# Kernel optimization log

Measured on AMD Instinct MI355X. Metric: run time of the kernel, lower is better.

## Reference

```python
import jax, jax.numpy as jnp
import numpy as np

# FP4 E2M1 value table (codes 0..7 positive, 8..15 negative, sign in MSB)
FP4_VALUES = jnp.array([0.0, 0.5, 1.0, 1.5, 2.0, 3.0, 4.0, 6.0,
                        -0.0, -0.5, -1.0, -1.5, -2.0, -3.0, -4.0, -6.0],
                       dtype=jnp.float32)


def setup_inputs() -> dict:
    key = jax.random.key(0)
    k1, k2, k3, k4 = jax.random.split(key, 4)
    O, I = 4096, 4096
    block = 16
    x = jax.random.normal(k1, (8192, I), dtype=jnp.float32)
    # packed uint4 pairs stored as int32 bytes in [0, 256)
    weight = jax.random.randint(k2, (O, I // 2), 0, 256, dtype=jnp.int32)
    # per-block FP8-style scales (positive)
    weight_scale = jax.random.uniform(k3, (O, I // block), dtype=jnp.float32, minval=0.01, maxval=1.0)
    bias = jax.random.normal(k4, (O,), dtype=jnp.float32)
    return {"x": x, "weight": weight, "weight_scale": weight_scale,
            "bias": bias, "block_size": block}


def _dequant_nvfp4(weight, weight_scale, block_size):
    # unpack two FP4 codes per byte: high nibble is the even (first) element
    hi = (weight >> 4) & 0xF
    lo = weight & 0xF
    O = weight.shape[0]
    codes = jnp.stack([hi, lo], axis=-1).reshape(O, -1)  # [O, I]
    vals = FP4_VALUES[codes]                             # [O, I] f32
    I = vals.shape[1]
    # apply per-block scale
    w = vals.reshape(O, I // block_size, block_size) * weight_scale[:, :, None]
    return w.reshape(O, I)


def reference(x, weight, weight_scale, bias, block_size):
    w = _dequant_nvfp4(weight, weight_scale, block_size)  # [O, I]
    return jnp.einsum('ti,oi->to', x, w) + bias[None, :]
```

## Files before the change

kernel.cpp:

```cpp
#include <hip/hip_runtime.h>
#include <hip/hip_fp16.h>

typedef __attribute__((ext_vector_type(8))) _Float16 f16x8;
typedef __attribute__((ext_vector_type(4))) float f32x4;

#define M_DIM 8192
#define N_DIM 4096
#define K_DIM 4096
#define BM 256
#define BN 256
#define BK 64
#define NT (K_DIM / BK)
#define ITERS (NT / 2)

__constant__ float FP4_LUT[16] = {0.f, 0.5f, 1.f, 1.5f, 2.f, 3.f, 4.f, 6.f,
                                  -0.f, -0.5f, -1.f, -1.5f, -2.f, -3.f, -4.f, -6.f};

__device__ inline void glds16(const void* g, void* l) {
    __builtin_amdgcn_global_load_lds(
        (const __attribute__((address_space(1))) void*)g,
        (__attribute__((address_space(3))) void*)l, 16, 0, 0);
}

__global__ __launch_bounds__(256) void prep_kernel(const float* __restrict__ x,
                                                   _Float16* __restrict__ xh,
                                                   const int* __restrict__ w,
                                                   const float* __restrict__ wsc,
                                                   _Float16* __restrict__ wh) {
    int b = blockIdx.x;
    if (b < 16384) {
        int i = (b * 256 + threadIdx.x) * 8;
        const float4* p = (const float4*)(x + i);
        float4 a = p[0], c = p[1];
        f16x8 h;
        h[0] = (_Float16)a.x; h[1] = (_Float16)a.y;
        h[2] = (_Float16)a.z; h[3] = (_Float16)a.w;
        h[4] = (_Float16)c.x; h[5] = (_Float16)c.y;
        h[6] = (_Float16)c.z; h[7] = (_Float16)c.w;
        *(f16x8*)(xh + i) = h;
    } else {
        int t = (b - 16384) * 256 + threadIdx.x;
        int4 b4 = ((const int4*)w)[t];
        int o  = t >> 9;
        int j0 = (t & 511) << 2;
        float s = wsc[(o << 8) + (j0 >> 3)];
        f16x8 h;
        int v;
        v = b4.x; h[0] = (_Float16)(FP4_LUT[(v >> 4) & 15] * s); h[1] = (_Float16)(FP4_LUT[v & 15] * s);
        v = b4.y; h[2] = (_Float16)(FP4_LUT[(v >> 4) & 15] * s); h[3] = (_Float16)(FP4_LUT[v & 15] * s);
        v = b4.z; h[4] = (_Float16)(FP4_LUT[(v >> 4) & 15] * s); h[5] = (_Float16)(FP4_LUT[v & 15] * s);
        v = b4.w; h[6] = (_Float16)(FP4_LUT[(v >> 4) & 15] * s); h[7] = (_Float16)(FP4_LUT[v & 15] * s);
        *(f16x8*)(wh + ((long)o << 12) + (j0 << 1)) = h;
    }
}


#define VM4 asm volatile("s_waitcnt vmcnt(4)" ::: "memory")
#define VM0 asm volatile("s_waitcnt vmcnt(0)" ::: "memory")
#define LG8 asm volatile("s_waitcnt lgkmcnt(8)" ::: "memory")
#define LG4 asm volatile("s_waitcnt lgkmcnt(4)" ::: "memory")
#define LG0 asm volatile("s_waitcnt lgkmcnt(0)" ::: "memory")
#define NOP ((void)0)

#define STAGE(OP, SD, KH, KOFF) do {                                           \
    _Float16* _d = lds + (SD)*32768 + (OP)*16384 + (KH)*8192 + (wid << 9);     \
    const _Float16* _s = ((OP) ? srcB : srcA) + (KOFF);                        \
    glds16(_s, _d);                                                            \
    glds16(_s + (size_t)128 * K_DIM, _d + 4096);                               \
  } while (0)

#define PH(DOAF, NCB, NKH, NMH, AFN, DOBF, BFN, LGW, MHC, AFC, BFC, STG, VMW, BAR) do { \
    STG;                                                                       \
    const _Float16* _nb = lds + (NCB)*32768 + (NKH)*8192;                      \
    if (DOAF) {                                                                \
      AFN[0] = *(const f16x8*)(_nb + a_off + (NMH)*2048);                      \
      AFN[1] = *(const f16x8*)(_nb + a_off + (NMH)*2048 + 512);                \
      AFN[2] = *(const f16x8*)(_nb + a_off + (NMH)*2048 + 1024);               \
      AFN[3] = *(const f16x8*)(_nb + a_off + (NMH)*2048 + 1536);               \
    }                                                                          \
    if (DOBF) {                                                                \
      BFN[0] = *(const f16x8*)(_nb + b_off);                                   \
      BFN[1] = *(const f16x8*)(_nb + b_off + 512);                             \
      BFN[2] = *(const f16x8*)(_nb + b_off + 1024);                            \
      BFN[3] = *(const f16x8*)(_nb + b_off + 1536);                            \
    }                                                                          \
    LGW;                                                                       \
    __builtin_amdgcn_s_setprio(1);                                             \
    _Pragma("unroll")                                                          \
    for (int mf = 0; mf < 4; ++mf) {                                           \
      _Pragma("unroll")                                                        \
      for (int nf = 0; nf < 4; ++nf)                                           \
        acc[(MHC)*4 + mf][nf] = __builtin_amdgcn_mfma_f32_16x16x32_f16(        \
            AFC[mf], BFC[nf], acc[(MHC)*4 + mf][nf], 0, 0, 0);                 \
    }                                                                          \
    __builtin_amdgcn_s_setprio(0);                                             \
    VMW;                                                                       \
    if (BAR) __builtin_amdgcn_s_barrier();                                     \
  } while (0)

__global__ __launch_bounds__(512, 2) void gemm_f16_pf(const _Float16* __restrict__ A,
                                                      const _Float16* __restrict__ B,
                                                      const float* __restrict__ bias,
                                                      float* __restrict__ C) {
    __shared__ _Float16 lds[2 * 32768];

    const int tid  = threadIdx.x;
    const int wid  = tid >> 6;
    const int lane = tid & 63;
    const int fr   = lane & 15;
    const int kg   = lane >> 4;
    const int wm   = wid >> 2;
    const int wn   = wid & 3;

    const int c = blockIdx.x & 7;
    const int q = blockIdx.x >> 3;
    const int bm = (c >> 1) * 8 + (q & 7);
    const int bn = (c & 1) * 8 + (q >> 3);
    const int brow = bm * BM;
    const int bcol = bn * BN;

    const int s_col = (((tid & 3) ^ ((tid >> 3) & 3)) << 3);
    const _Float16* srcA = A + (size_t)(brow + (tid >> 2)) * K_DIM + s_col;
    const _Float16* srcB = B + (size_t)(bcol + (tid >> 2)) * K_DIM + s_col;

    const int swz   = ((kg ^ ((fr >> 1) & 3)) << 3);
    const int a_off = (wm * 128 + fr) * 32 + swz;
    const int b_off = 16384 + (wn * 64 + fr) * 32 + swz;

    f16x8 af0[4], af1[4], bf0[4], bf1[4];
    f32x4 acc[8][4] = {};

    STAGE(0, 0, 0, 0);
    STAGE(1, 0, 0, 0);
    STAGE(0, 0, 1, 32);
    STAGE(1, 0, 1, 32);
    STAGE(0, 1, 0, 64);
    STAGE(1, 1, 0, 64);
    VM4;
    __builtin_amdgcn_s_barrier();
    af0[0] = *(const f16x8*)(lds + a_off);
    af0[1] = *(const f16x8*)(lds + a_off + 512);
    af0[2] = *(const f16x8*)(lds + a_off + 1024);
    af0[3] = *(const f16x8*)(lds + a_off + 1536);
    bf0[0] = *(const f16x8*)(lds + b_off);
    bf0[1] = *(const f16x8*)(lds + b_off + 512);
    bf0[2] = *(const f16x8*)(lds + b_off + 1024);
    bf0[3] = *(const f16x8*)(lds + b_off + 1536);

    for (int i = 0; i < ITERS - 1; ++i) {
        const int kb = i << 7;
        PH(1, 0,0,1, af1, 0,bf0, LG4, 0, af0, bf0, STAGE(0,1,1,kb+96),  NOP, 0);
        PH(1, 0,1,0, af0, 1,bf1, LG8, 1, af1, bf0, STAGE(1,1,1,kb+96),  VM4, 1);
        PH(1, 0,1,1, af1, 0,bf0, LG4, 0, af0, bf1, STAGE(0,0,0,kb+128), NOP, 0);
        PH(1, 1,0,0, af0, 1,bf0, LG8, 1, af1, bf1, STAGE(1,0,0,kb+128), VM4, 1);
        PH(1, 1,0,1, af1, 0,bf0, LG4, 0, af0, bf0, STAGE(0,0,1,kb+160), NOP, 0);
        PH(1, 1,1,0, af0, 1,bf1, LG8, 1, af1, bf0, STAGE(1,0,1,kb+160), VM4, 1);
        PH(1, 1,1,1, af1, 0,bf0, LG4, 0, af0, bf1, STAGE(0,1,0,kb+192), NOP, 0);
        PH(1, 0,0,0, af0, 1,bf0, LG8, 1, af1, bf1, STAGE(1,1,0,kb+192), VM4, 1);
    }
    {
        const int kb = (ITERS - 1) << 7;
        PH(1, 0,0,1, af1, 0,bf0, LG4, 0, af0, bf0, STAGE(0,1,1,kb+96), NOP, 0);
        PH(1, 0,1,0, af0, 1,bf1, LG8, 1, af1, bf0, STAGE(1,1,1,kb+96), VM4, 1);
        PH(1, 0,1,1, af1, 0,bf0, LG4, 0, af0, bf1, NOP,                NOP, 0);
        PH(1, 1,0,0, af0, 1,bf0, LG8, 1, af1, bf1, NOP,                VM0, 1);
        PH(1, 1,0,1, af1, 0,bf0, LG4, 0, af0, bf0, NOP,                NOP, 0);
        PH(1, 1,1,0, af0, 1,bf1, LG8, 1, af1, bf0, NOP,                NOP, 1);
        PH(1, 1,1,1, af1, 0,bf0, LG4, 0, af0, bf1, NOP,                NOP, 0);
        PH(0, 0,0,0, af0, 0,bf0, LG0, 1, af1, bf1, NOP,                NOP, 0);
    }

#pragma unroll
    for (int m = 0; m < 8; ++m) {
        int row = brow + wm * 128 + m * 16 + kg * 4;
#pragma unroll
        for (int n = 0; n < 4; ++n) {
            int col = bcol + wn * 64 + n * 16 + fr;
            float bv = bias[col];
#pragma unroll
            for (int j = 0; j < 4; ++j)
                C[(size_t)(row + j) * N_DIM + col] = acc[m][n][j] + bv;
        }
    }
}

__global__ __launch_bounds__(256) void fallback_kernel(const float* __restrict__ x,
                                                       const int* __restrict__ w,
                                                       const float* __restrict__ wsc,
                                                       const float* __restrict__ bias,
                                                       float* __restrict__ out) {
    long idx = (long)blockIdx.x * 256 + threadIdx.x;
    int t = (int)(idx >> 12);
    int o = (int)(idx & 4095);
    float acc = 0.f;
    for (int j = 0; j < K_DIM / 2; ++j) {
        int b = w[o * (K_DIM / 2) + j];
        float s = wsc[(o << 8) + (j >> 3)];
        acc += x[(long)t * K_DIM + 2 * j]     * (FP4_LUT[(b >> 4) & 15] * s);
        acc += x[(long)t * K_DIM + 2 * j + 1] * (FP4_LUT[b & 15] * s);
    }
    out[idx] = acc + bias[o];
}

extern "C" void kernel_launch(void* const* d_in, const int* in_sizes, int n_in,
                              void* d_out, int out_size, void* d_ws, size_t ws_size,
                              hipStream_t stream) {
    const float* x    = (const float*)d_in[0];
    const int*   w    = (const int*)d_in[1];
    const float* wsc  = (const float*)d_in[2];
    const float* bias = (const float*)d_in[3];
    float* out = (float*)d_out;

    const size_t xh_bytes = (size_t)M_DIM * K_DIM * 2;
    const size_t wh_bytes = (size_t)N_DIM * K_DIM * 2;

    if (ws_size >= xh_bytes + wh_bytes) {
        _Float16* xh = (_Float16*)d_ws;
        _Float16* wh = (_Float16*)((char*)d_ws + xh_bytes);
        prep_kernel<<<16384 + 8192, 256, 0, stream>>>(x, xh, w, wsc, wh);
        gemm_f16_pf<<<(M_DIM / BM) * (N_DIM / BN), 512, 0, stream>>>(xh, wh, bias, out);
    } else {
        fallback_kernel<<<((long)M_DIM * N_DIM) / 256, 256, 0, stream>>>(x, w, wsc, bias, out);
    }
}
```

Measured before the change: 276.6 us.

## Switch GEMM inner loop from 16x16x32 to 32x32x16 MFMA tiles

```diff
diff --git a/kernel.cpp b/kernel.cpp
--- a/kernel.cpp
+++ b/kernel.cpp
@@ -2,7 +2,7 @@
 #include <hip/hip_fp16.h>
 
 typedef __attribute__((ext_vector_type(8))) _Float16 f16x8;
-typedef __attribute__((ext_vector_type(4))) float f32x4;
+typedef __attribute__((ext_vector_type(16))) float f32x16;
 
 #define M_DIM 8192
 #define N_DIM 4096
@@ -87,12 +87,13 @@
     LGW;                                                                       \
     __builtin_amdgcn_s_setprio(1);                                             \
     _Pragma("unroll")                                                          \
-    for (int mf = 0; mf < 4; ++mf) {                                           \
+    for (int ks = 0; ks < 2; ++ks)                                             \
       _Pragma("unroll")                                                        \
-      for (int nf = 0; nf < 4; ++nf)                                           \
-        acc[(MHC)*4 + mf][nf] = __builtin_amdgcn_mfma_f32_16x16x32_f16(        \
-            AFC[mf], BFC[nf], acc[(MHC)*4 + mf][nf], 0, 0, 0);                 \
-    }                                                                          \
+      for (int ms = 0; ms < 2; ++ms)                                           \
+        _Pragma("unroll")                                                      \
+        for (int ns = 0; ns < 2; ++ns)                                         \
+          acc[(MHC)*2 + ms][ns] = __builtin_amdgcn_mfma_f32_32x32x16_f16(      \
+              AFC[ms*2+ks], BFC[ns*2+ks], acc[(MHC)*2 + ms][ns], 0, 0, 0);     \
     __builtin_amdgcn_s_setprio(0);                                             \
     VMW;                                                                       \
     if (BAR) __builtin_amdgcn_s_barrier();                                     \
@@ -107,8 +108,8 @@
     const int tid  = threadIdx.x;
     const int wid  = tid >> 6;
     const int lane = tid & 63;
-    const int fr   = lane & 15;
-    const int kg   = lane >> 4;
+    const int l31  = lane & 31;
+    const int hh   = lane >> 5;
     const int wm   = wid >> 2;
     const int wn   = wid & 3;
 
@@ -119,16 +120,17 @@
     const int brow = bm * BM;
     const int bcol = bn * BN;
 
-    const int s_col = (((tid & 3) ^ ((tid >> 3) & 3)) << 3);
-    const _Float16* srcA = A + (size_t)(brow + (tid >> 2)) * K_DIM + s_col;
-    const _Float16* srcB = B + (size_t)(bcol + (tid >> 2)) * K_DIM + s_col;
-
-    const int swz   = ((kg ^ ((fr >> 1) & 3)) << 3);
-    const int a_off = (wm * 128 + fr) * 32 + swz;
-    const int b_off = 16384 + (wn * 64 + fr) * 32 + swz;
+    const int s_row = ((tid >> 7) << 5) + ((tid >> 1) & 31);
+    const int s_k   = (((tid >> 6) & 1) << 4) + ((tid & 1) << 3);
+    const _Float16* srcA = A + (size_t)(brow + s_row) * K_DIM + s_k;
+    const _Float16* srcB = B + (size_t)(bcol + s_row) * K_DIM + s_k;
+
+    const int lane_off = (l31 << 4) + (hh << 3);
+    const int a_off = (wm << 12) + lane_off;
+    const int b_off = 16384 + (wn << 11) + lane_off;
 
     f16x8 af0[4], af1[4], bf0[4], bf1[4];
-    f32x4 acc[8][4] = {};
+    f32x16 acc[4][2] = {};
 
     STAGE(0, 0, 0, 0);
     STAGE(1, 0, 0, 0);
@@ -171,15 +173,17 @@
     }
 
 #pragma unroll
-    for (int m = 0; m < 8; ++m) {
-        int row = brow + wm * 128 + m * 16 + kg * 4;
+    for (int mi = 0; mi < 4; ++mi) {
+        int rbase = brow + wm * 128 + mi * 32 + 4 * hh;
 #pragma unroll
-        for (int n = 0; n < 4; ++n) {
-            int col = bcol + wn * 64 + n * 16 + fr;
+        for (int ni = 0; ni < 2; ++ni) {
+            int col = bcol + wn * 64 + ni * 32 + l31;
             float bv = bias[col];
 #pragma unroll
-            for (int j = 0; j < 4; ++j)
-                C[(size_t)(row + j) * N_DIM + col] = acc[m][n][j] + bv;
+            for (int j = 0; j < 16; ++j) {
+                int row = rbase + (j & 3) + 8 * (j >> 2);
+                C[(size_t)row * N_DIM + col] = acc[mi][ni][j] + bv;
+            }
         }
     }
 }
```

New measurement: 304.6 us. 1.1x slower.
